# Performance work log

Hardware: AMD Instinct MI355X
Metric: run time of the kernel (lower is better)

Reference implementation:

```python
import jax, jax.numpy as jnp
import numpy as np

B, S, D = 4, 2048, 1024
H = 16
KD = 1024  # key_dim (total)
VD = 1024  # value_dim (total)


def setup_inputs() -> dict:
    key = jax.random.key(0)
    ks = jax.random.split(key, 8)
    queries = jax.random.normal(ks[0], (B, S, D), dtype=jnp.float32)
    keys_ = jax.random.normal(ks[1], (B, S, D), dtype=jnp.float32)
    values = jax.random.normal(ks[2], (B, S, D), dtype=jnp.float32)
    # causal float mask (1 = keep, 0 = masked), broadcasts over [B, H, S, S]
    mask = jnp.tril(jnp.ones((S, S), dtype=jnp.float32))[None, None]
    # Linear weights stored as [in, out] so forward is x @ W
    Wq = jax.random.normal(ks[3], (D, KD), dtype=jnp.float32) / np.sqrt(D)
    Wk = jax.random.normal(ks[4], (D, KD), dtype=jnp.float32) / np.sqrt(D)
    Wv = jax.random.normal(ks[5], (D, VD), dtype=jnp.float32) / np.sqrt(D)
    Wo = jax.random.normal(ks[6], (H * VD // H * H // H * 1 if False else VD, D), dtype=jnp.float32) / np.sqrt(VD)
    bo = jnp.zeros((D,), dtype=jnp.float32)
    return {"queries": queries, "keys": keys_, "values": values, "mask": mask,
            "Wq": Wq, "Wk": Wk, "Wv": Wv, "Wo": Wo, "bo": bo}


def reference(queries, keys, values, mask, Wq, Wk, Wv, Wo, bo):
    b, s, _ = queries.shape
    # project then split heads: [B, S, H, hd] -> [B, H, S, hd]
    q = (queries @ Wq).reshape(b, s, H, -1).transpose(0, 2, 1, 3)
    k = (keys @ Wk).reshape(b, s, H, -1).transpose(0, 2, 1, 3)
    v = (values @ Wv).reshape(b, s, H, -1).transpose(0, 2, 1, 3)
    dk = k.shape[-1]  # per-head key dim (scale uses post-split dk, as in source)
    logits = jnp.einsum('bhqd,bhkd->bhqk', q, k) / jnp.sqrt(jnp.float32(dk))
    logits = logits + (1.0 - mask) * (-1e9)
    attn = jax.nn.softmax(logits, axis=-1)  # dropout p=0 in eval -> identity
    o = jnp.einsum('bhqk,bhkd->bhqd', attn, v)
    o = o.transpose(0, 2, 1, 3).reshape(b, s, H * (VD // H))
    return o @ Wo + bo
```

## Files before the change

kernel.cpp:

```cpp
#include <hip/hip_runtime.h>
#include <hip/hip_bf16.h>

typedef __attribute__((ext_vector_type(8))) short s8v;
typedef __attribute__((ext_vector_type(4))) short s4v;
typedef __attribute__((ext_vector_type(4))) float f4v;

#define S_LEN 2048
#define NH 16
#define HD 64
#define DMODEL 1024
#define KVB 64
#define LOG2E 1.44269504088896f
#define FIXMAX 32.0f

__device__ __forceinline__ unsigned short f2bf(float f) {
  union { float f; unsigned int u; } v; v.f = f;
  return (unsigned short)((v.u + 0x7FFFu + ((v.u >> 16) & 1u)) >> 16);
}

__device__ __forceinline__ f4v mfma16(s8v a, s8v b, f4v c) {
  return __builtin_amdgcn_mfma_f32_16x16x32_bf16(a, b, c, 0, 0, 0);
}

__device__ __forceinline__ void gl_lds16(const unsigned short* g, unsigned short* l) {
  __builtin_amdgcn_global_load_lds(
      (const __attribute__((address_space(1))) void*)g,
      (__attribute__((address_space(3))) void*)l, 16, 0, 0);
}

__global__ __launch_bounds__(256)
void cast3(const float* __restrict__ a, const float* __restrict__ b,
           const float* __restrict__ c, unsigned short* __restrict__ oa,
           unsigned short* __restrict__ ob, unsigned short* __restrict__ oc,
           int n8) {
  const float* src = (blockIdx.y == 0) ? a : (blockIdx.y == 1) ? b : c;
  unsigned short* dst = (blockIdx.y == 0) ? oa : (blockIdx.y == 1) ? ob : oc;
  for (int i = blockIdx.x * 256 + threadIdx.x; i < n8; i += gridDim.x * 256) {
    f4v v0 = *(const f4v*)(src + (size_t)i * 8);
    f4v v1 = *(const f4v*)(src + (size_t)i * 8 + 4);
    unsigned short cv[8];
#pragma unroll
    for (int j = 0; j < 4; j++) { cv[j] = f2bf(v0[j]); cv[4 + j] = f2bf(v1[j]); }
    *(s8v*)(dst + (size_t)i * 8) = *(const s8v*)cv;
  }
}

__global__ __launch_bounds__(256)
void transpose_cast4(const float* __restrict__ w0, const float* __restrict__ w1,
                     const float* __restrict__ w2, const float* __restrict__ w3,
                     unsigned short* __restrict__ o0, unsigned short* __restrict__ o1,
                     unsigned short* __restrict__ o2, unsigned short* __restrict__ o3) {
  __shared__ float tile[32][33];
  const int z = blockIdx.z;
  const float* W = (z == 0) ? w0 : (z == 1) ? w1 : (z == 2) ? w2 : w3;
  unsigned short* Wt = (z == 0) ? o0 : (z == 1) ? o1 : (z == 2) ? o2 : o3;
  int x = threadIdx.x, y = threadIdx.y;
  int n0 = blockIdx.x * 32, k0 = blockIdx.y * 32;
#pragma unroll
  for (int i = 0; i < 32; i += 8)
    tile[y + i][x] = W[(size_t)(k0 + y + i) * DMODEL + n0 + x];
  __syncthreads();
#pragma unroll
  for (int i = 0; i < 32; i += 8)
    Wt[(size_t)(n0 + y + i) * DMODEL + k0 + x] = f2bf(tile[x][y + i]);
}

template <typename Epi>
__device__ __forceinline__ void gemm_body(const unsigned short* __restrict__ A_,
                                          const unsigned short* __restrict__ Bt_,
                                          Epi epi) {
  __shared__ unsigned short As[128 * 64];
  __shared__ unsigned short Bs[128 * 64];
  const int t = threadIdx.x;
  const int l = t & 63;
  const int w = t >> 6, wr = w >> 1, wc = w & 1;
  const int m0 = blockIdx.x * 128, n0 = blockIdx.y * 128;
  const int lg = l >> 4, lm = l & 15;

  f4v acc[4][4];
#pragma unroll
  for (int i = 0; i < 4; i++)
#pragma unroll
    for (int j = 0; j < 4; j++) acc[i][j] = f4v{0.f, 0.f, 0.f, 0.f};

  const int sgc = (l & 7) ^ ((l >> 3) & 7);
  const unsigned short* Aprow = A_ + (size_t)(m0 + w * 8 + (l >> 3)) * DMODEL + sgc * 8;
  const unsigned short* Bprow = Bt_ + (size_t)(n0 + w * 8 + (l >> 3)) * DMODEL + sgc * 8;
  const int xo0 = (lg ^ (lm & 7)) << 4;
  const int xo1 = ((4 + lg) ^ (lm & 7)) << 4;

  for (int k0 = 0; k0 < DMODEL; k0 += 64) {
#pragma unroll
    for (int i = 0; i < 4; i++) {
      gl_lds16(Aprow + (size_t)(i * 32) * DMODEL + k0, &As[i * 2048 + w * 512]);
      gl_lds16(Bprow + (size_t)(i * 32) * DMODEL + k0, &Bs[i * 2048 + w * 512]);
    }
    __syncthreads();

    s8v af[4][2], bf[4][2];
#pragma unroll
    for (int mi = 0; mi < 4; mi++) {
      const char* ar = (const char*)As + (wr * 64 + mi * 16 + lm) * 128;
      af[mi][0] = *(const s8v*)(ar + xo0);
      af[mi][1] = *(const s8v*)(ar + xo1);
    }
#pragma unroll
    for (int ni = 0; ni < 4; ni++) {
      const char* br = (const char*)Bs + (wc * 64 + ni * 16 + lm) * 128;
      bf[ni][0] = *(const s8v*)(br + xo0);
      bf[ni][1] = *(const s8v*)(br + xo1);
    }
#pragma unroll
    for (int mi = 0; mi < 4; mi++)
#pragma unroll
      for (int ni = 0; ni < 4; ni++) {
        acc[mi][ni] = mfma16(af[mi][0], bf[ni][0], acc[mi][ni]);
        acc[mi][ni] = mfma16(af[mi][1], bf[ni][1], acc[mi][ni]);
      }
    __syncthreads();
  }
  epi(acc, m0, n0, wr, wc, lg, lm);
}

__global__ __launch_bounds__(256, 2)
void qkv_gemm(const unsigned short* __restrict__ Qc, const unsigned short* __restrict__ Kc,
              const unsigned short* __restrict__ Vc, const unsigned short* __restrict__ WqT,
              const unsigned short* __restrict__ WkT, const unsigned short* __restrict__ WvT,
              unsigned short* __restrict__ Qb, unsigned short* __restrict__ Kb,
              unsigned short* __restrict__ Vtb) {
  const int z = blockIdx.z;
  const unsigned short* A = (z == 0) ? Qc : (z == 1) ? Kc : Vc;
  const unsigned short* Bt = (z == 0) ? WqT : (z == 1) ? WkT : WvT;
  unsigned short* C = (z == 0) ? Qb : (z == 1) ? Kb : Vtb;
  const float scale = (z == 0) ? 0.125f * LOG2E : 1.0f;

  gemm_body(A, Bt, [&](f4v (&acc)[4][4], int m0, int n0, int wr, int wc,
                       int lg, int lm) {
#pragma unroll
    for (int mi = 0; mi < 4; mi++)
#pragma unroll
      for (int ni = 0; ni < 4; ni++) {
        int col = n0 + wc * 64 + ni * 16 + lm;
#pragma unroll
        for (int rr = 0; rr < 4; rr++) {
          int row = m0 + wr * 64 + mi * 16 + lg * 4 + rr;
          unsigned short h = f2bf(acc[mi][ni][rr] * scale);
          int b = row >> 11, s = row & 2047, hh = col >> 6, d = col & 63;
          if (z < 2)
            C[(((size_t)(b * NH + hh)) * S_LEN + s) * HD + d] = h;
          else
            C[(((size_t)(b * NH + hh)) * HD + d) * S_LEN + s] = h;
        }
      }
  });
}

__global__ __launch_bounds__(256, 2)
void out_gemm(const unsigned short* __restrict__ A, const unsigned short* __restrict__ Bt,
              float* __restrict__ Cp, const float* __restrict__ bias) {
  gemm_body(A, Bt, [&](f4v (&acc)[4][4], int m0, int n0, int wr, int wc,
                       int lg, int lm) {
#pragma unroll
    for (int mi = 0; mi < 4; mi++)
#pragma unroll
      for (int ni = 0; ni < 4; ni++) {
        int col = n0 + wc * 64 + ni * 16 + lm;
        float bv = bias[col];
#pragma unroll
        for (int rr = 0; rr < 4; rr++) {
          int row = m0 + wr * 64 + mi * 16 + lg * 4 + rr;
          Cp[(size_t)row * DMODEL + col] = acc[mi][ni][rr] + bv;
        }
      }
  });
}

__global__ __launch_bounds__(256, 2)
void attn_k(const unsigned short* __restrict__ Q, const unsigned short* __restrict__ Km,
            const unsigned short* __restrict__ Vt, unsigned short* __restrict__ O) {
  __shared__ unsigned short Ks[2][KVB * HD];
  __shared__ unsigned short Vs[2][HD * KVB];
  __shared__ unsigned short pbuf[16][16 * KVB];
  const int t = threadIdx.x, l = t & 63, w = t >> 6;
  const int lg = l >> 4, lm = l & 15;

  const int c = blockIdx.x;
  const int bh = c & 63;
  const int pr4 = (c >> 6) & 3;
  const int pr = (c >> 8) ? 7 - pr4 : pr4;
  const int s0A = (15 - pr) * 128, s0B = pr * 128;

  const unsigned short* Qh = Q + (size_t)bh * S_LEN * HD;
  const unsigned short* Kh = Km + (size_t)bh * S_LEN * HD;
  const unsigned short* Vh = Vt + (size_t)bh * HD * S_LEN;

  const int xo0 = (lg ^ (lm & 7)) << 4;
  const int xo1 = ((4 + lg) ^ (lm & 7)) << 4;

  const int q00 = s0A + w * 32, q01 = q00 + 16;
  const int q02 = s0B + w * 32, q03 = q02 + 16;

  s8v qf0[2], qf1[2], qf2[2], qf3[2];
#define LOADQ(QF, Q0)                                                   \
  QF[0] = *(const s8v*)(Qh + (size_t)((Q0) + lm) * HD + lg * 8);        \
  QF[1] = *(const s8v*)(Qh + (size_t)((Q0) + lm) * HD + 32 + lg * 8);
  LOADQ(qf0, q00) LOADQ(qf1, q01) LOADQ(qf2, q02) LOADQ(qf3, q03)
#undef LOADQ

  f4v o0[4], o1[4], o2[4], o3[4];
#pragma unroll
  for (int i = 0; i < 4; i++) {
    o0[i] = f4v{0.f, 0.f, 0.f, 0.f}; o1[i] = f4v{0.f, 0.f, 0.f, 0.f};
    o2[i] = f4v{0.f, 0.f, 0.f, 0.f}; o3[i] = f4v{0.f, 0.f, 0.f, 0.f};
  }
  float l0_ = 0.f, l1_ = 0.f, l2_ = 0.f, l3_ = 0.f;

  const int sr0 = w * 8 + (l >> 3);
  const int sj = l & 7;

#define STAGE(buf, kv)                                                          \
  {                                                                             \
    _Pragma("unroll")                                                           \
    for (int i = 0; i < 2; i++) {                                               \
      int r_ = sr0 + i * 32;                                                    \
      int jj_ = ((sj ^ (r_ & 7)) << 3);                                         \
      gl_lds16(Kh + (size_t)((kv) + r_) * HD + jj_, &Ks[buf][w * 512 + i * 2048]); \
      gl_lds16(Vh + (size_t)r_ * S_LEN + (kv) + jj_, &Vs[buf][w * 512 + i * 2048]); \
    }                                                                           \
  }

#define TILE_S(QF, LL, Q0, PI)                                                  \
  {                                                                             \
    const int dt = (Q0) >> 6;                                                   \
    if (ti <= dt) {                                                             \
      f4v s_[4];                                                                \
      _Pragma("unroll")                                                         \
      for (int sub = 0; sub < 4; sub++) {                                       \
        s_[sub] = f4v{0.f, 0.f, 0.f, 0.f};                                      \
        s_[sub] = mfma16(kf[sub * 2], QF[0], s_[sub]);                          \
        s_[sub] = mfma16(kf[sub * 2 + 1], QF[1], s_[sub]);                      \
      }                                                                         \
      if (ti == dt) {                                                           \
        const int qrow = (Q0) + lm;                                             \
        _Pragma("unroll")                                                       \
        for (int sub = 0; sub < 4; sub++) {                                     \
          const int kbase = kv + sub * 16 + lg * 4;                             \
          _Pragma("unroll")                                                     \
          for (int rr = 0; rr < 4; rr++)                                        \
            if (kbase + rr > qrow) s_[sub][rr] = -1e30f;                        \
        }                                                                       \
      }                                                                         \
      char* pb_ = (char*)pbuf[w * 4 + PI];                                      \
      float psum = 0.f;                                                         \
      _Pragma("unroll")                                                         \
      for (int sub = 0; sub < 4; sub++) {                                       \
        float p0 = exp2f(s_[sub][0] - FIXMAX);                                  \
        float p1 = exp2f(s_[sub][1] - FIXMAX);                                  \
        float p2 = exp2f(s_[sub][2] - FIXMAX);                                  \
        float p3 = exp2f(s_[sub][3] - FIXMAX);                                  \
        psum += (p0 + p1) + (p2 + p3);                                          \
        unsigned int u01, u23;                                                  \
        asm("v_cvt_pk_bf16_f32 %0, %1, %2" : "=v"(u01) : "v"(p0), "v"(p1));     \
        asm("v_cvt_pk_bf16_f32 %0, %1, %2" : "=v"(u23) : "v"(p2), "v"(p3));     \
        const int cc = (sub * 4 + lg) ^ ((lm & 7) << 1);                        \
        uint2 pv; pv.x = u01; pv.y = u23;                                       \
        *(uint2*)(pb_ + lm * 128 + (cc << 3)) = pv;                             \
      }                                                                         \
      (LL) += psum;                                                             \
    }                                                                           \
  }

#define TILE_PV(OO, Q0, PI)                                                     \
  {                                                                             \
    const int dt = (Q0) >> 6;                                                   \
    if (ti <= dt) {                                                             \
      const char* pb_ = (const char*)pbuf[w * 4 + PI];                          \
      s8v pf0 = *(const s8v*)(pb_ + lm * 128 + xo0);                            \
      s8v pf1 = *(const s8v*)(pb_ + lm * 128 + xo1);                            \
      _Pragma("unroll")                                                         \
      for (int nc = 0; nc < 4; nc++) {                                          \
        OO[nc] = mfma16(vf[nc * 2], pf0, OO[nc]);                               \
        OO[nc] = mfma16(vf[nc * 2 + 1], pf1, OO[nc]);                           \
      }                                                                         \
    }                                                                           \
  }

  const int nt = 2 * (15 - pr) + 2;
  int cur = 0;
  STAGE(0, 0);
  __syncthreads();

  for (int ti = 0; ti < nt; ++ti) {
    const int kv = ti * 64;
    if (ti + 1 < nt) STAGE(cur ^ 1, kv + 64);

    const unsigned short* Kb = Ks[cur];
    const unsigned short* Vb = Vs[cur];

    s8v kf[8];
#pragma unroll
    for (int sub = 0; sub < 4; sub++) {
      const char* krow = (const char*)Kb + (sub * 16 + lm) * 128;
      kf[sub * 2] = *(const s8v*)(krow + xo0);
      kf[sub * 2 + 1] = *(const s8v*)(krow + xo1);
    }

    TILE_S(qf0, l0_, q00, 0);
    TILE_S(qf1, l1_, q01, 1);
    TILE_S(qf2, l2_, q02, 2);
    TILE_S(qf3, l3_, q03, 3);

    __builtin_amdgcn_sched_barrier(0);

    s8v vf[8];
#pragma unroll
    for (int sub = 0; sub < 4; sub++) {
      const char* vrow = (const char*)Vb + (sub * 16 + lm) * 128;
      vf[sub * 2] = *(const s8v*)(vrow + xo0);
      vf[sub * 2 + 1] = *(const s8v*)(vrow + xo1);
    }

    TILE_PV(o0, q00, 0);
    TILE_PV(o1, q01, 1);
    TILE_PV(o2, q02, 2);
    TILE_PV(o3, q03, 3);

    __syncthreads();
    cur ^= 1;
  }

  const int b = bh >> 4, hh = bh & 15;
#define EPI(OO, LL, Q0)                                                         \
  {                                                                             \
    float lt = (LL);                                                            \
    lt += __shfl_xor(lt, 16);                                                   \
    lt += __shfl_xor(lt, 32);                                                   \
    const float inv = 1.f / lt;                                                 \
    unsigned short* Orow =                                                      \
        O + ((size_t)b * S_LEN + (Q0) + lm) * DMODEL + hh * HD;                 \
    _Pragma("unroll")                                                           \
    for (int nc = 0; nc < 4; nc++) {                                            \
      unsigned short h4[4];                                                     \
      _Pragma("unroll")                                                         \
      for (int rr = 0; rr < 4; rr++) h4[rr] = f2bf(OO[nc][rr] * inv);           \
      *(s4v*)(Orow + nc * 16 + lg * 4) = *(const s4v*)h4;                       \
    }                                                                           \
  }
  EPI(o0, l0_, q00);
  EPI(o1, l1_, q01);
  EPI(o2, l2_, q02);
  EPI(o3, l3_, q03);
#undef EPI
#undef TILE_PV
#undef TILE_S
#undef STAGE
}

extern "C" void kernel_launch(void* const* d_in, const int* in_sizes, int n_in,
                              void* d_out, int out_size, void* d_ws, size_t ws_size,
                              hipStream_t stream) {
  const float* queries = (const float*)d_in[0];
  const float* keys = (const float*)d_in[1];
  const float* values = (const float*)d_in[2];
  const float* Wq = (const float*)d_in[4];
  const float* Wk = (const float*)d_in[5];
  const float* Wv = (const float*)d_in[6];
  const float* Wo = (const float*)d_in[7];
  const float* bo = (const float*)d_in[8];

  char* ws = (char*)d_ws;
  const size_t WB = (size_t)DMODEL * DMODEL * 2;
  unsigned short* WqT = (unsigned short*)(ws + 0 * WB);
  unsigned short* WkT = (unsigned short*)(ws + 1 * WB);
  unsigned short* WvT = (unsigned short*)(ws + 2 * WB);
  unsigned short* WoT = (unsigned short*)(ws + 3 * WB);
  const size_t TB = (size_t)4 * S_LEN * DMODEL * 2;
  unsigned short* Qb  = (unsigned short*)(ws + 4 * WB);
  unsigned short* Kb  = (unsigned short*)(ws + 4 * WB + TB);
  unsigned short* Vtb = (unsigned short*)(ws + 4 * WB + 2 * TB);
  unsigned short* Ob  = (unsigned short*)(ws + 4 * WB + 3 * TB);
  unsigned short* Qc  = (unsigned short*)(ws + 4 * WB + 4 * TB);
  unsigned short* Kc  = (unsigned short*)(ws + 4 * WB + 5 * TB);
  unsigned short* Vc  = (unsigned short*)(ws + 4 * WB + 6 * TB);

  const int M = 4 * S_LEN;

  cast3<<<dim3(2048, 3), 256, 0, stream>>>(queries, keys, values, Qc, Kc, Vc,
                                           M * DMODEL / 8);

  transpose_cast4<<<dim3(32, 32, 4), dim3(32, 8), 0, stream>>>(
      Wq, Wk, Wv, Wo, WqT, WkT, WvT, WoT);

  qkv_gemm<<<dim3(64, 8, 3), 256, 0, stream>>>(Qc, Kc, Vc, WqT, WkT, WvT,
                                               Qb, Kb, Vtb);

  attn_k<<<512, 256, 0, stream>>>(Qb, Kb, Vtb, Ob);

  out_gemm<<<dim3(64, 8), 256, 0, stream>>>(Ob, WoT, (float*)d_out, bo);
}
```

Baseline: 185.4 us.

## Triple-buffer K/V tiles and prefetch next K fragments into registers

```diff
diff --git a/kernel.cpp b/kernel.cpp
--- a/kernel.cpp
+++ b/kernel.cpp
@@ -178,8 +178,8 @@
 __global__ __launch_bounds__(256, 2)
 void attn_k(const unsigned short* __restrict__ Q, const unsigned short* __restrict__ Km,
             const unsigned short* __restrict__ Vt, unsigned short* __restrict__ O) {
-  __shared__ unsigned short Ks[2][KVB * HD];
-  __shared__ unsigned short Vs[2][HD * KVB];
+  __shared__ unsigned short Ks[3][KVB * HD];
+  __shared__ unsigned short Vs[3][HD * KVB];
   __shared__ unsigned short pbuf[16][16 * KVB];
   const int t = threadIdx.x, l = t & 63, w = t >> 6;
   const int lg = l >> 4, lm = l & 15;
@@ -229,7 +229,17 @@
     }                                                                           \
   }
 
-#define TILE_S(QF, LL, Q0, PI)                                                  \
+#define LOADKF(DST, SRC)                                                        \
+  {                                                                             \
+    _Pragma("unroll")                                                           \
+    for (int sub = 0; sub < 4; sub++) {                                         \
+      const char* krow_ = (const char*)(SRC) + (sub * 16 + lm) * 128;           \
+      DST[sub * 2] = *(const s8v*)(krow_ + xo0);                                \
+      DST[sub * 2 + 1] = *(const s8v*)(krow_ + xo1);                            \
+    }                                                                           \
+  }
+
+#define TILE_S(KF, QF, LL, Q0, PI)                                              \
   {                                                                             \
     const int dt = (Q0) >> 6;                                                   \
     if (ti <= dt) {                                                             \
@@ -237,8 +247,8 @@
       _Pragma("unroll")                                                         \
       for (int sub = 0; sub < 4; sub++) {                                       \
         s_[sub] = f4v{0.f, 0.f, 0.f, 0.f};                                      \
-        s_[sub] = mfma16(kf[sub * 2], QF[0], s_[sub]);                          \
-        s_[sub] = mfma16(kf[sub * 2 + 1], QF[1], s_[sub]);                      \
+        s_[sub] = mfma16(KF[sub * 2], QF[0], s_[sub]);                          \
+        s_[sub] = mfma16(KF[sub * 2 + 1], QF[1], s_[sub]);                      \
       }                                                                         \
       if (ti == dt) {                                                           \
         const int qrow = (Q0) + lm;                                             \
@@ -285,48 +295,43 @@
     }                                                                           \
   }
 
+#define STEP(TI, KC, KN)                                                        \
+  {                                                                             \
+    const int ti = (TI);                                                        \
+    const int kv = ti * 64;                                                     \
+    if (ti + 2 < nt) STAGE((ti + 2) % 3, kv + 128);                             \
+    const unsigned short* Vb = Vs[ti % 3];                                      \
+    s8v vf[8];                                                                  \
+    _Pragma("unroll")                                                           \
+    for (int sub = 0; sub < 4; sub++) {                                         \
+      const char* vrow_ = (const char*)Vb + (sub * 16 + lm) * 128;              \
+      vf[sub * 2] = *(const s8v*)(vrow_ + xo0);                                 \
+      vf[sub * 2 + 1] = *(const s8v*)(vrow_ + xo1);                             \
+    }                                                                           \
+    if (ti + 1 < nt) LOADKF(KN, Ks[(ti + 1) % 3]);                              \
+    TILE_S(KC, qf0, l0_, q00, 0);                                               \
+    TILE_S(KC, qf1, l1_, q01, 1);                                               \
+    TILE_S(KC, qf2, l2_, q02, 2);                                               \
+    TILE_S(KC, qf3, l3_, q03, 3);                                               \
+    __builtin_amdgcn_sched_barrier(0);                                          \
+    TILE_PV(o0, q00, 0);                                                        \
+    TILE_PV(o1, q01, 1);                                                        \
+    TILE_PV(o2, q02, 2);                                                        \
+    TILE_PV(o3, q03, 3);                                                        \
+    __syncthreads();                                                            \
+  }
+
   const int nt = 2 * (15 - pr) + 2;
-  int cur = 0;
   STAGE(0, 0);
+  STAGE(1, 64);
   __syncthreads();
 
-  for (int ti = 0; ti < nt; ++ti) {
-    const int kv = ti * 64;
-    if (ti + 1 < nt) STAGE(cur ^ 1, kv + 64);
-
-    const unsigned short* Kb = Ks[cur];
-    const unsigned short* Vb = Vs[cur];
-
-    s8v kf[8];
-#pragma unroll
-    for (int sub = 0; sub < 4; sub++) {
-      const char* krow = (const char*)Kb + (sub * 16 + lm) * 128;
-      kf[sub * 2] = *(const s8v*)(krow + xo0);
-      kf[sub * 2 + 1] = *(const s8v*)(krow + xo1);
-    }
-
-    TILE_S(qf0, l0_, q00, 0);
-    TILE_S(qf1, l1_, q01, 1);
-    TILE_S(qf2, l2_, q02, 2);
-    TILE_S(qf3, l3_, q03, 3);
-
-    __builtin_amdgcn_sched_barrier(0);
-
-    s8v vf[8];
-#pragma unroll
-    for (int sub = 0; sub < 4; sub++) {
-      const char* vrow = (const char*)Vb + (sub * 16 + lm) * 128;
-      vf[sub * 2] = *(const s8v*)(vrow + xo0);
-      vf[sub * 2 + 1] = *(const s8v*)(vrow + xo1);
-    }
-
-    TILE_PV(o0, q00, 0);
-    TILE_PV(o1, q01, 1);
-    TILE_PV(o2, q02, 2);
-    TILE_PV(o3, q03, 3);
-
-    __syncthreads();
-    cur ^= 1;
+  s8v kfA[8], kfB[8];
+  LOADKF(kfA, Ks[0]);
+
+  for (int ti2 = 0; ti2 < nt; ti2 += 2) {
+    STEP(ti2, kfA, kfB);
+    STEP(ti2 + 1, kfB, kfA);
   }
 
   const int b = bh >> 4, hh = bh & 15;
@@ -351,8 +356,10 @@
   EPI(o2, l2_, q02);
   EPI(o3, l3_, q03);
 #undef EPI
+#undef STEP
 #undef TILE_PV
 #undef TILE_S
+#undef LOADKF
 #undef STAGE
 }
 
```

New measurement: 189.7 us. 2.3% more time.
